# Kernel optimization log

Measured on AMD Instinct MI355X. Metric: run time of the kernel, lower is better.

The kernel has to match this reference:

```python
import jax, jax.numpy as jnp
import numpy as np

N_NODES = 50000
N_EDGES = 800000
B = 512
DIM_IN = 128
D2 = 200
D3 = 200
GC1 = 100
DG = 20
DH = 64
H1 = 128
H2 = 32
BN_EPS = 1e-5


def _lin_init(k, fan_in, fan_out):
    s = 1.0 / np.sqrt(fan_in)
    kw, kb = jax.random.split(k)
    W = jax.random.uniform(kw, (fan_in, fan_out), jnp.float32, -s, s)
    b = jax.random.uniform(kb, (fan_out,), jnp.float32, -s, s)
    return W, b


def setup_inputs() -> dict:
    key = jax.random.key(0)
    ks = jax.random.split(key, 16)
    feat = jax.random.normal(ks[0], (N_NODES, DIM_IN), jnp.float32)
    desc_2d = jax.random.normal(ks[1], (B, D2), jnp.float32)
    desc_3d = jax.random.normal(ks[2], (B, D3), jnp.float32)
    src = jax.random.randint(ks[3], (N_EDGES,), 0, N_NODES, jnp.int32)
    dst = jax.random.randint(ks[4], (N_EDGES,), 0, N_NODES, jnp.int32)
    graph_id = jnp.sort(jax.random.randint(ks[5], (N_NODES,), 0, B, jnp.int32))
    gc1_W, gc1_b = _lin_init(ks[6], DIM_IN, GC1)
    gc2_W, gc2_b = _lin_init(ks[7], GC1, DG)
    pg_W, pg_b = _lin_init(ks[8], DG, DH)
    p2_W, p2_b = _lin_init(ks[9], D2, DH)
    # xavier_uniform for W2
    lim = np.sqrt(6.0 / (DH + DH))
    W2 = jax.random.uniform(ks[10], (DH, DH), jnp.float32, -lim, lim)
    fusion_dim = (DG + 1) * (D2 + 1)
    fc1_W, fc1_b = _lin_init(ks[11], fusion_dim, H1)
    fc2_W, fc2_b = _lin_init(ks[12], H1, H2)
    fc3_W, fc3_b = _lin_init(ks[13], H2, 1)
    return {
        'feat': feat, 'desc_2d': desc_2d, 'desc_3d': desc_3d,
        'gc1_W': gc1_W, 'gc1_b': gc1_b, 'gc2_W': gc2_W, 'gc2_b': gc2_b,
        'pg_W': pg_W, 'pg_b': pg_b, 'p2_W': p2_W, 'p2_b': p2_b, 'W2': W2,
        'fc1_W': fc1_W, 'fc1_b': fc1_b, 'fc2_W': fc2_W, 'fc2_b': fc2_b,
        'fc3_W': fc3_W, 'fc3_b': fc3_b,
        'bn1_g': jnp.ones((H1,), jnp.float32), 'bn1_b': jnp.zeros((H1,), jnp.float32),
        'bn2_g': jnp.ones((H2,), jnp.float32), 'bn2_b': jnp.zeros((H2,), jnp.float32),
        'src': src, 'dst': dst, 'graph_id': graph_id,
    }


def _gcn(h, src, dst, W, b):
    # copy_u -> mean over incoming mailbox -> linear apply
    agg = jax.ops.segment_sum(h[src], dst, num_segments=N_NODES)
    deg = jax.ops.segment_sum(jnp.ones((src.shape[0],), h.dtype), dst, num_segments=N_NODES)
    h_mean = agg / jnp.maximum(deg, 1.0)[:, None]  # zero in-degree -> 0 (DGL default)
    return h_mean @ W + b


def _bn(x, g, b):
    mu = x.mean(0)
    var = x.var(0)
    return (x - mu) * jax.lax.rsqrt(var + BN_EPS) * g + b


def reference(feat, desc_2d, desc_3d, gc1_W, gc1_b, gc2_W, gc2_b,
              pg_W, pg_b, p2_W, p2_b, W2,
              fc1_W, fc1_b, fc2_W, fc2_b, fc3_W, fc3_b,
              bn1_g, bn1_b, bn2_g, bn2_b, src, dst, graph_id):
    h = jax.nn.relu(_gcn(feat, src, dst, gc1_W, gc1_b))          # [N, 100]
    h = jax.nn.relu(_gcn(h, src, dst, gc2_W, gc2_b))             # [N, 20]
    # dgl.mean_nodes: per-graph mean of node features
    cnt = jax.ops.segment_sum(jnp.ones((N_NODES,), h.dtype), graph_id, num_segments=B)
    hg = jax.ops.segment_sum(h, graph_id, num_segments=B) / jnp.maximum(cnt, 1.0)[:, None]  # [B, 20]
    h_g = hg @ pg_W + pg_b                                        # [B, 64]
    h_d = desc_2d @ p2_W + p2_b                                   # [B, 64]
    s = ((h_g @ W2) * h_d).sum(-1)                                # [B]
    a = jax.nn.sigmoid(s)[:, None]                                # [B, 1]
    ones = jnp.ones((B, 1), hg.dtype)
    hg1 = jnp.concatenate([hg, ones], axis=1)                     # [B, 21]
    d1 = jnp.concatenate([a * desc_2d, ones], axis=1)             # [B, 201]
    fusion = (hg1[:, :, None] * d1[:, None, :]).reshape(B, -1)    # [B, 21*201]
    out = jax.nn.relu(_bn(fusion @ fc1_W + fc1_b, bn1_g, bn1_b))
    out = jax.nn.relu(_bn(out @ fc2_W + fc2_b, bn2_g, bn2_b))
    return out @ fc3_W + fc3_b                                    # [B, 1]
```

## Files before the change

### kernel.cpp

```cpp
#include <hip/hip_runtime.h>

#define NN 50000
#define NE 800000
#define NB 512
#define DIN 128
#define DD2 200
#define C1 100
#define C2 20
#define DHH 64
#define HH1 128
#define HH2 32
#define KD 201
#define KDP 204
#define NU 2688
#define SCB 196
#define NCT 7
#define NTILE 3125
#define GB1 782
#define FPB 3125
#define FCB 672
#define PS1 128
#define SLOT 32
#define OVFCAP 8192
#define CSTR 16

typedef short sh8 __attribute__((ext_vector_type(8)));
typedef float f32x4 __attribute__((ext_vector_type(4)));

__device__ __forceinline__ unsigned short f2bf(float x) {
    unsigned u = __float_as_uint(x);
    unsigned r = (u + 0x7fffu + ((u >> 16) & 1u)) >> 16;
    return (unsigned short)r;
}
__device__ __forceinline__ float bf_lo(unsigned u) { return __uint_as_float(u << 16); }
__device__ __forceinline__ float bf_hi(unsigned u) { return __uint_as_float(u & 0xffff0000u); }

__global__ void k_packB_init(const float* __restrict__ W, unsigned short* __restrict__ Bf,
                             int* __restrict__ cnt, float* __restrict__ hgs,
                             int* __restrict__ ovfc) {
    int idx = blockIdx.x * 256 + threadIdx.x;
    if (idx < NCT * 4 * 64) {
        int lane = idx & 63;
        int kc = (idx >> 6) & 3;
        int ct = idx >> 8;
        int col = ct * 16 + (lane & 15);
        int k0 = kc * 32 + (lane >> 4) * 8;
        unsigned short* outp = Bf + (size_t)idx * 8;
        #pragma unroll
        for (int e = 0; e < 8; ++e) {
            float v = (col < C1) ? W[(k0 + e) * C1 + col] : 0.f;
            outp[e] = f2bf(v);
        }
    }
    for (int i = idx; i < NN * CSTR; i += SCB * 256) cnt[i] = 0;
    if (idx < NB * C2) hgs[idx] = 0.f;
    if (idx == 0) *ovfc = 0;
}

__global__ __launch_bounds__(256) void k_front(const float* __restrict__ feat,
                                               const unsigned short* __restrict__ Bf,
                                               unsigned char* __restrict__ t1f8,
                                               const int* __restrict__ src,
                                               const int* __restrict__ dst,
                                               int* __restrict__ cnt,
                                               unsigned short* __restrict__ epad,
                                               int2* __restrict__ ovf,
                                               int* __restrict__ ovfc,
                                               const float* __restrict__ desc2d,
                                               const float* __restrict__ W1,
                                               float* __restrict__ V) {
    __shared__ float smem[7168];
    const int tid = threadIdx.x;

    if (blockIdx.x >= GB1 + FCB) {
        int e = (blockIdx.x - GB1 - FCB) * 256 + tid;
        if (e < NE) {
            int d = dst[e], s = src[e];
            int slot = atomicAdd(&cnt[d * CSTR], 1);
            if (slot < SLOT) {
                epad[(size_t)d * SLOT + slot] = (unsigned short)s;
            } else {
                int o = atomicAdd(ovfc, 1);
                if (o < OVFCAP) ovf[o] = make_int2(d, s);
            }
        }
        return;
    }

    if (blockIdx.x < GB1) {
        sh8* sB = (sh8*)smem;
        {
            const uint4* srcp = (const uint4*)Bf;
            uint4* dstp = (uint4*)smem;
            for (int i = tid; i < NCT * 4 * 64; i += 256) dstp[i] = srcp[i];
        }
        __syncthreads();
        const int w = tid >> 6, lane = tid & 63;
        const int ri = lane & 15;
        const int kg = lane >> 4;
        int tile = blockIdx.x * 4 + w;
        if (tile < NTILE) {
            const int n = tile * 16 + ri;
            f32x4 acc[NCT];
            #pragma unroll
            for (int ct = 0; ct < NCT; ++ct) acc[ct] = (f32x4){0.f, 0.f, 0.f, 0.f};
            #pragma unroll
            for (int kc = 0; kc < 4; ++kc) {
                const float* ap = feat + (size_t)n * DIN + kc * 32 + kg * 8;
                float4 a0 = *(const float4*)ap;
                float4 a1 = *(const float4*)(ap + 4);
                union { sh8 v; unsigned short u[8]; } af;
                af.u[0] = f2bf(a0.x); af.u[1] = f2bf(a0.y);
                af.u[2] = f2bf(a0.z); af.u[3] = f2bf(a0.w);
                af.u[4] = f2bf(a1.x); af.u[5] = f2bf(a1.y);
                af.u[6] = f2bf(a1.z); af.u[7] = f2bf(a1.w);
                #pragma unroll
                for (int ct = 0; ct < NCT; ++ct)
                    acc[ct] = __builtin_amdgcn_mfma_f32_16x16x32_bf16(
                        af.v, sB[(ct * 4 + kc) * 64 + lane], acc[ct], 0, 0, 0);
            }
            const int rbase = tile * 16 + kg * 4;
            #pragma unroll
            for (int ct = 0; ct < NCT; ++ct) {
                int col = ct * 16 + ri;
                if (col < C1) {
                    #pragma unroll
                    for (int r = 0; r < 4; ++r) {
                        int pk = __builtin_amdgcn_cvt_pk_fp8_f32(acc[ct][r], acc[ct][r], 0, false);
                        t1f8[(size_t)(rbase + r) * PS1 + col] = (unsigned char)(pk & 0xFF);
                    }
                }
            }
        }
        return;
    }

    {
        float (*S)[KDP] = (float(*)[KDP])smem;
        int fid = blockIdx.x - GB1;
        const int i = fid / 32;
        const int rem = fid % 32;
        const int bt = rem >> 1;
        const int half = rem & 1;
        for (int idx = tid; idx < 32 * 50; idx += 256) {
            int r = idx / 50, c4 = idx % 50;
            *(float4*)&S[r][c4 * 4] =
                *(const float4*)(desc2d + (size_t)(bt * 32 + r) * DD2 + c4 * 4);
        }
        __syncthreads();
        const int c = tid & 31;
        const int rg = tid >> 5;
        float acc[4][2];
        #pragma unroll
        for (int r = 0; r < 4; ++r) { acc[r][0] = 0.f; acc[r][1] = 0.f; }
        const float* Wb = W1 + (size_t)i * (KD * HH1) + half * 64 + c;
        for (int k = 0; k < 200; k += 4) {
            const float* Wk = Wb + (size_t)k * HH1;
            float w0[2], w1[2], w2[2], w3[2];
            #pragma unroll
            for (int m = 0; m < 2; ++m) {
                w0[m] = Wk[32 * m];
                w1[m] = Wk[HH1 + 32 * m];
                w2[m] = Wk[2 * HH1 + 32 * m];
                w3[m] = Wk[3 * HH1 + 32 * m];
            }
            #pragma unroll
            for (int r = 0; r < 4; ++r) {
                float4 a4 = *(const float4*)&S[rg * 4 + r][k];
                #pragma unroll
                for (int m = 0; m < 2; ++m)
                    acc[r][m] += a4.x * w0[m] + a4.y * w1[m] + a4.z * w2[m] + a4.w * w3[m];
            }
        }
        #pragma unroll
        for (int r = 0; r < 4; ++r) {
            int b = bt * 32 + rg * 4 + r;
            float* Vr = V + (size_t)b * NU + i * HH1 + half * 64 + c;
            Vr[0] = acc[r][0];
            Vr[32] = acc[r][1];
        }
    }
}

__global__ __launch_bounds__(256) void k_agg1(const unsigned char* __restrict__ t1f8,
                                              const int* __restrict__ cnt,
                                              const unsigned short* __restrict__ epad,
                                              const int2* __restrict__ ovf,
                                              const int* __restrict__ ovfc,
                                              const float* __restrict__ b1,
                                              unsigned* __restrict__ h1b) {
    const int tid = threadIdx.x;
    const int w = tid >> 6, l = tid & 63;
    const int n = blockIdx.x * 4 + w;
    if (n >= NN || l >= 50) return;
    const int deg = cnt[n * CSTR];
    const int m = deg < SLOT ? deg : SLOT;
    const unsigned short* ep = epad + (size_t)n * SLOT;
    const int co = 2 * l;
    float acc0 = 0.f, acc1 = 0.f;
    int e = 0;
    for (; e + 7 < m; e += 8) {
        int s0 = ep[e],     s1 = ep[e + 1], s2 = ep[e + 2], s3 = ep[e + 3];
        int s4 = ep[e + 4], s5 = ep[e + 5], s6 = ep[e + 6], s7 = ep[e + 7];
        int u0 = *(const unsigned short*)(t1f8 + (size_t)s0 * PS1 + co);
        int u1 = *(const unsigned short*)(t1f8 + (size_t)s1 * PS1 + co);
        int u2 = *(const unsigned short*)(t1f8 + (size_t)s2 * PS1 + co);
        int u3 = *(const unsigned short*)(t1f8 + (size_t)s3 * PS1 + co);
        int u4 = *(const unsigned short*)(t1f8 + (size_t)s4 * PS1 + co);
        int u5 = *(const unsigned short*)(t1f8 + (size_t)s5 * PS1 + co);
        int u6 = *(const unsigned short*)(t1f8 + (size_t)s6 * PS1 + co);
        int u7 = *(const unsigned short*)(t1f8 + (size_t)s7 * PS1 + co);
        acc0 += __builtin_amdgcn_cvt_f32_fp8(u0, 0); acc1 += __builtin_amdgcn_cvt_f32_fp8(u0, 1);
        acc0 += __builtin_amdgcn_cvt_f32_fp8(u1, 0); acc1 += __builtin_amdgcn_cvt_f32_fp8(u1, 1);
        acc0 += __builtin_amdgcn_cvt_f32_fp8(u2, 0); acc1 += __builtin_amdgcn_cvt_f32_fp8(u2, 1);
        acc0 += __builtin_amdgcn_cvt_f32_fp8(u3, 0); acc1 += __builtin_amdgcn_cvt_f32_fp8(u3, 1);
        acc0 += __builtin_amdgcn_cvt_f32_fp8(u4, 0); acc1 += __builtin_amdgcn_cvt_f32_fp8(u4, 1);
        acc0 += __builtin_amdgcn_cvt_f32_fp8(u5, 0); acc1 += __builtin_amdgcn_cvt_f32_fp8(u5, 1);
        acc0 += __builtin_amdgcn_cvt_f32_fp8(u6, 0); acc1 += __builtin_amdgcn_cvt_f32_fp8(u6, 1);
        acc0 += __builtin_amdgcn_cvt_f32_fp8(u7, 0); acc1 += __builtin_amdgcn_cvt_f32_fp8(u7, 1);
    }
    for (; e < m; ++e) {
        int u = *(const unsigned short*)(t1f8 + (size_t)ep[e] * PS1 + co);
        acc0 += __builtin_amdgcn_cvt_f32_fp8(u, 0);
        acc1 += __builtin_amdgcn_cvt_f32_fp8(u, 1);
    }
    if (deg > SLOT) {
        int novf = *ovfc; novf = novf < OVFCAP ? novf : OVFCAP;
        for (int j2 = 0; j2 < novf; ++j2) {
            int2 p = ovf[j2];
            if (p.x == n) {
                int u = *(const unsigned short*)(t1f8 + (size_t)p.y * PS1 + co);
                acc0 += __builtin_amdgcn_cvt_f32_fp8(u, 0);
                acc1 += __builtin_amdgcn_cvt_f32_fp8(u, 1);
            }
        }
    }
    float d = (float)(deg > 0 ? deg : 1);
    float v0 = fmaxf(acc0 / d + b1[co], 0.f);
    float v1 = fmaxf(acc1 / d + b1[co + 1], 0.f);
    h1b[(size_t)n * 50 + l] = (unsigned)f2bf(v0) | ((unsigned)f2bf(v1) << 16);
}

__global__ void k_gemm2(const unsigned* __restrict__ h1b, const float* __restrict__ W,
                        unsigned* __restrict__ t2b) {
    __shared__ float sW[C1 * C2];
    __shared__ float sr[16][C1];
    __shared__ float sc[16][C2];
    for (int idx = threadIdx.x; idx < C1 * C2; idx += 320) sW[idx] = W[idx];
    int ln = threadIdx.x / C2, j = threadIdx.x % C2;
    int n0 = blockIdx.x * 16;
    for (int idx = threadIdx.x; idx < 16 * 50; idx += 320) {
        int r = idx / 50, c = idx % 50;
        int n = n0 + r;
        unsigned u = (n < NN) ? h1b[(size_t)n * 50 + c] : 0u;
        sr[r][2 * c] = bf_lo(u);
        sr[r][2 * c + 1] = bf_hi(u);
    }
    __syncthreads();
    if (ln < 16) {
        float acc = 0.f;
        #pragma unroll 4
        for (int k = 0; k < C1; ++k) acc += sr[ln][k] * sW[k * C2 + j];
        sc[ln][j] = acc;
    }
    __syncthreads();
    for (int idx = threadIdx.x; idx < 16 * 10; idx += 320) {
        int r = idx / 10, jp = idx % 10;
        int n = n0 + r;
        if (n < NN)
            t2b[(size_t)n * 10 + jp] =
                (unsigned)f2bf(sc[r][2 * jp]) | ((unsigned)f2bf(sc[r][2 * jp + 1]) << 16);
    }
}

__global__ void k_agg2p(const unsigned* __restrict__ t2b, const int* __restrict__ cnt,
                        const unsigned short* __restrict__ epad, const int2* __restrict__ ovf,
                        const int* __restrict__ ovfc, const float* __restrict__ bias,
                        const int* __restrict__ gid, float* __restrict__ hgs) {
    int ln = threadIdx.x / C2, c = threadIdx.x % C2;
    if (ln >= 12) return;
    int n = blockIdx.x * 12 + ln;
    if (n >= NN) return;
    const int deg = cnt[n * CSTR];
    const int m = deg < SLOT ? deg : SLOT;
    const unsigned short* ep = epad + (size_t)n * SLOT;
    const int jp = c >> 1, hi = c & 1;
    float acc = 0.f;
    int e = 0;
    for (; e + 3 < m; e += 4) {
        int s0 = ep[e], s1 = ep[e + 1], s2 = ep[e + 2], s3 = ep[e + 3];
        unsigned u0 = t2b[(size_t)s0 * 10 + jp];
        unsigned u1 = t2b[(size_t)s1 * 10 + jp];
        unsigned u2 = t2b[(size_t)s2 * 10 + jp];
        unsigned u3 = t2b[(size_t)s3 * 10 + jp];
        acc += hi ? bf_hi(u0) : bf_lo(u0);
        acc += hi ? bf_hi(u1) : bf_lo(u1);
        acc += hi ? bf_hi(u2) : bf_lo(u2);
        acc += hi ? bf_hi(u3) : bf_lo(u3);
    }
    for (; e < m; ++e) {
        unsigned u = t2b[(size_t)ep[e] * 10 + jp];
        acc += hi ? bf_hi(u) : bf_lo(u);
    }
    if (deg > SLOT) {
        int novf = *ovfc; novf = novf < OVFCAP ? novf : OVFCAP;
        for (int j2 = 0; j2 < novf; ++j2) {
            int2 p = ovf[j2];
            if (p.x == n) {
                unsigned u = t2b[(size_t)p.y * 10 + jp];
                acc += hi ? bf_hi(u) : bf_lo(u);
            }
        }
    }
    float d = (float)(deg > 0 ? deg : 1);
    float v = acc / d + bias[c];
    v = v > 0.f ? v : 0.f;
    atomicAdd(&hgs[gid[n] * C2 + c], v);
}

__global__ __launch_bounds__(128) void k_hfc1(const float* __restrict__ hgs,
                                              const int* __restrict__ gid,
                                              const float* __restrict__ desc2d,
                                              const float* __restrict__ pgW,
                                              const float* __restrict__ pgb,
                                              const float* __restrict__ p2W,
                                              const float* __restrict__ p2b,
                                              const float* __restrict__ W2,
                                              const float* __restrict__ V,
                                              const float* __restrict__ W1,
                                              float* __restrict__ o1) {
    __shared__ float shg[C2];
    __shared__ float sg[DHH];
    __shared__ float sa;
    const int b = blockIdx.x, tid = threadIdx.x;
    if (tid < C2) {
        int lo = 0, hi = NN;
        while (lo < hi) { int m = (lo + hi) >> 1; if (gid[m] < b) lo = m + 1; else hi = m; }
        int lo2 = lo, hi2 = NN;
        while (lo2 < hi2) { int m = (lo2 + hi2) >> 1; if (gid[m] < b + 1) lo2 = m + 1; else hi2 = m; }
        float dcnt = (float)(lo2 - lo);
        if (dcnt < 1.f) dcnt = 1.f;
        shg[tid] = hgs[b * C2 + tid] / dcnt;
    }
    __syncthreads();
    float hdj = 0.f;
    if (tid < DHH) {
        float hgj = pgb[tid];
        #pragma unroll
        for (int k = 0; k < C2; ++k) hgj += shg[k] * pgW[k * DHH + tid];
        hdj = p2b[tid];
        #pragma unroll 4
        for (int k = 0; k < DD2; ++k) hdj += desc2d[b * DD2 + k] * p2W[k * DHH + tid];
        sg[tid] = hgj;
    }
    __syncthreads();
    if (tid < DHH) {
        float tj = 0.f;
        #pragma unroll 4
        for (int k = 0; k < DHH; ++k) tj += sg[k] * W2[k * DHH + tid];
        float v = tj * hdj;
        #pragma unroll
        for (int off = 32; off; off >>= 1) v += __shfl_xor(v, off, 64);
        if (tid == 0) sa = 1.f / (1.f + expf(-v));
    }
    __syncthreads();
    const int j = tid;
    const float* Vb = V + (size_t)b * NU + j;
    const float* WL = W1 + (size_t)200 * HH1 + j;
    float sv = Vb[20 * HH1];
    float sw = WL[(size_t)20 * KD * HH1];
    #pragma unroll
    for (int i = 0; i < 20; ++i) {
        float h = shg[i];
        sv += h * Vb[i * HH1];
        sw += h * WL[(size_t)i * KD * HH1];
    }
    o1[b * HH1 + j] = sa * sv + sw;
}

__global__ __launch_bounds__(128) void k_fc2s(const float* __restrict__ o1,
                                              const float* __restrict__ g,
                                              const float* __restrict__ beta,
                                              const float* __restrict__ W,
                                              float* __restrict__ o2) {
    __shared__ float r[HH1];
    __shared__ float part[4][HH2];
    const int tid = threadIdx.x;
    float s = 0.f, s2 = 0.f;
    for (int b = 0; b < NB; ++b) {
        float v = o1[b * HH1 + tid];
        s += v; s2 += v * v;
    }
    float mu = s / NB;
    float rstd = rsqrtf(s2 / NB - mu * mu + 1e-5f);
    float scale = rstd * g[tid];
    float shift = beta[tid] - mu * scale;
    const int m = tid & 31, p = tid >> 5;
    for (int q = 0; q < 4; ++q) {
        int b = blockIdx.x * 4 + q;
        float v = o1[b * HH1 + tid];
        __syncthreads();
        r[tid] = fmaxf(v * scale + shift, 0.f);
        __syncthreads();
        float acc = 0.f;
        #pragma unroll 4
        for (int j = p * 32; j < p * 32 + 32; ++j) acc += r[j] * W[j * HH2 + m];
        part[p][m] = acc;
        __syncthreads();
        if (tid < HH2) o2[b * HH2 + tid] = part[0][tid] + part[1][tid] + part[2][tid] + part[3][tid];
    }
}

__global__ __launch_bounds__(512) void k_finals(const float* __restrict__ o2,
                                                const float* __restrict__ g,
                                                const float* __restrict__ beta,
                                                const float* __restrict__ W3,
                                                const float* __restrict__ b3,
                                                float* __restrict__ out) {
    __shared__ float ps[16][HH2], ps2[16][HH2];
    __shared__ float sscale[HH2], sshift[HH2];
    const int tid = threadIdx.x;
    const int gq = tid >> 5, m = tid & 31;
    float s = 0.f, s2 = 0.f;
    for (int rr = 0; rr < 32; ++rr) {
        float v = o2[(gq * 32 + rr) * HH2 + m];
        s += v; s2 += v * v;
    }
    ps[gq][m] = s; ps2[gq][m] = s2;
    __syncthreads();
    if (tid < HH2) {
        float ts = 0.f, ts2 = 0.f;
        #pragma unroll
        for (int q = 0; q < 16; ++q) { ts += ps[q][tid]; ts2 += ps2[q][tid]; }
        float mu = ts / NB;
        float rstd = rsqrtf(ts2 / NB - mu * mu + 1e-5f);
        float scale = rstd * g[tid];
        sscale[tid] = scale;
        sshift[tid] = beta[tid] - mu * scale;
    }
    __syncthreads();
    float acc = b3[0];
    #pragma unroll 4
    for (int mm = 0; mm < HH2; ++mm) {
        float v = o2[tid * HH2 + mm];
        acc += fmaxf(v * sscale[mm] + sshift[mm], 0.f) * W3[mm];
    }
    out[tid] = acc;
}

extern "C" void kernel_launch(void* const* d_in, const int* in_sizes, int n_in,
                              void* d_out, int out_size, void* d_ws, size_t ws_size,
                              hipStream_t stream) {
    const float* feat   = (const float*)d_in[0];
    const float* desc2d = (const float*)d_in[1];
    const float* gc1W = (const float*)d_in[3];
    const float* gc1b = (const float*)d_in[4];
    const float* gc2W = (const float*)d_in[5];
    const float* gc2b = (const float*)d_in[6];
    const float* pgW  = (const float*)d_in[7];
    const float* pgb  = (const float*)d_in[8];
    const float* p2W  = (const float*)d_in[9];
    const float* p2b  = (const float*)d_in[10];
    const float* W2   = (const float*)d_in[11];
    const float* fc1W = (const float*)d_in[12];
    const float* fc2W = (const float*)d_in[14];
    const float* fc3W = (const float*)d_in[16];
    const float* fc3b = (const float*)d_in[17];
    const float* bn1g = (const float*)d_in[18];
    const float* bn1b = (const float*)d_in[19];
    const float* bn2g = (const float*)d_in[20];
    const float* bn2b = (const float*)d_in[21];
    const int* src = (const int*)d_in[22];
    const int* dst = (const int*)d_in[23];
    const int* gid = (const int*)d_in[24];
    float* out = (float*)d_out;

    char* ws = (char*)d_ws;
    size_t off = 0;
    auto alloc = [&](size_t nb) {
        void* p = ws + off;
        off = (off + nb + 255) & ~(size_t)255;
        return p;
    };
    unsigned char* t1f8 = (unsigned char*)alloc((size_t)NN * PS1);
    unsigned* h1b = (unsigned*)alloc((size_t)NN * 50 * 4);
    unsigned* t2b = (unsigned*)alloc((size_t)NN * 10 * 4);
    int* cnt_in  = (int*)alloc((size_t)NN * CSTR * 4);
    unsigned short* epad = (unsigned short*)alloc((size_t)NN * SLOT * 2);
    int2* ovf    = (int2*)alloc((size_t)OVFCAP * 8);
    int* ovfc    = (int*)alloc(256);
    unsigned short* Bf = (unsigned short*)alloc((size_t)NCT * 4 * 64 * 16);
    float* V     = (float*)alloc((size_t)NB * NU * 4);
    float* hgs   = (float*)alloc((size_t)NB * C2 * 4);
    float* o1    = (float*)alloc((size_t)NB * HH1 * 4);
    float* o2    = (float*)alloc((size_t)NB * HH2 * 4);

    k_packB_init<<<SCB, 256, 0, stream>>>(gc1W, Bf, cnt_in, hgs, ovfc);
    k_front<<<GB1 + FCB + FPB, 256, 0, stream>>>(feat, Bf, t1f8, src, dst, cnt_in,
                                                 epad, ovf, ovfc, desc2d, fc1W, V);

    k_agg1<<<(NN + 3) / 4, 256, 0, stream>>>(t1f8, cnt_in, epad, ovf, ovfc, gc1b, h1b);
    k_gemm2<<<(NN + 15) / 16, 320, 0, stream>>>(h1b, gc2W, t2b);
    k_agg2p<<<(NN + 11) / 12, 256, 0, stream>>>(t2b, cnt_in, epad, ovf, ovfc, gc2b, gid, hgs);

    k_hfc1<<<NB, 128, 0, stream>>>(hgs, gid, desc2d, pgW, pgb, p2W, p2b, W2, V, fc1W, o1);
    k_fc2s<<<NB / 4, 128, 0, stream>>>(o1, bn1g, bn1b, fc2W, o2);
    k_finals<<<1, 512, 0, stream>>>(o2, bn2g, bn2b, fc3W, fc3b, out);
}
```

Before: 182.6 us.

## Fuse layer-1 neighbor aggregation with layer-2 GEMM in one kernel

Merges the first GCN aggregation kernel and the 100x20 projection GEMM into one kernel. Each 1024-thread block aggregates 16 nodes into shared memory, then multiplies them by the shared-memory copy of W2 and writes the bf16 outputs. This removes the h1b intermediate buffer's global write and read and one kernel launch. The cost is large blocks with a barrier, which may hurt occupancy and latency hiding in the gather-bound aggregation, and each block reloads W2.

```diff
diff --git a/kernel.cpp b/kernel.cpp
--- a/kernel.cpp
+++ b/kernel.cpp
@@ -182,94 +182,81 @@
     }
 }
 
-__global__ __launch_bounds__(256) void k_agg1(const unsigned char* __restrict__ t1f8,
-                                              const int* __restrict__ cnt,
-                                              const unsigned short* __restrict__ epad,
-                                              const int2* __restrict__ ovf,
-                                              const int* __restrict__ ovfc,
-                                              const float* __restrict__ b1,
-                                              unsigned* __restrict__ h1b) {
+__global__ __launch_bounds__(1024) void k_agg1g2(const unsigned char* __restrict__ t1f8,
+                                                 const int* __restrict__ cnt,
+                                                 const unsigned short* __restrict__ epad,
+                                                 const int2* __restrict__ ovf,
+                                                 const int* __restrict__ ovfc,
+                                                 const float* __restrict__ b1,
+                                                 const float* __restrict__ W2,
+                                                 unsigned* __restrict__ t2b) {
+    __shared__ float sW2[C1 * C2];
+    __shared__ float sh1[16][C1];
+    __shared__ float sc[16][C2];
     const int tid = threadIdx.x;
+    for (int idx = tid; idx < C1 * C2; idx += 1024) sW2[idx] = W2[idx];
     const int w = tid >> 6, l = tid & 63;
-    const int n = blockIdx.x * 4 + w;
-    if (n >= NN || l >= 50) return;
-    const int deg = cnt[n * CSTR];
-    const int m = deg < SLOT ? deg : SLOT;
-    const unsigned short* ep = epad + (size_t)n * SLOT;
-    const int co = 2 * l;
-    float acc0 = 0.f, acc1 = 0.f;
-    int e = 0;
-    for (; e + 7 < m; e += 8) {
-        int s0 = ep[e],     s1 = ep[e + 1], s2 = ep[e + 2], s3 = ep[e + 3];
-        int s4 = ep[e + 4], s5 = ep[e + 5], s6 = ep[e + 6], s7 = ep[e + 7];
-        int u0 = *(const unsigned short*)(t1f8 + (size_t)s0 * PS1 + co);
-        int u1 = *(const unsigned short*)(t1f8 + (size_t)s1 * PS1 + co);
-        int u2 = *(const unsigned short*)(t1f8 + (size_t)s2 * PS1 + co);
-        int u3 = *(const unsigned short*)(t1f8 + (size_t)s3 * PS1 + co);
-        int u4 = *(const unsigned short*)(t1f8 + (size_t)s4 * PS1 + co);
-        int u5 = *(const unsigned short*)(t1f8 + (size_t)s5 * PS1 + co);
-        int u6 = *(const unsigned short*)(t1f8 + (size_t)s6 * PS1 + co);
-        int u7 = *(const unsigned short*)(t1f8 + (size_t)s7 * PS1 + co);
-        acc0 += __builtin_amdgcn_cvt_f32_fp8(u0, 0); acc1 += __builtin_amdgcn_cvt_f32_fp8(u0, 1);
-        acc0 += __builtin_amdgcn_cvt_f32_fp8(u1, 0); acc1 += __builtin_amdgcn_cvt_f32_fp8(u1, 1);
-        acc0 += __builtin_amdgcn_cvt_f32_fp8(u2, 0); acc1 += __builtin_amdgcn_cvt_f32_fp8(u2, 1);
-        acc0 += __builtin_amdgcn_cvt_f32_fp8(u3, 0); acc1 += __builtin_amdgcn_cvt_f32_fp8(u3, 1);
-        acc0 += __builtin_amdgcn_cvt_f32_fp8(u4, 0); acc1 += __builtin_amdgcn_cvt_f32_fp8(u4, 1);
-        acc0 += __builtin_amdgcn_cvt_f32_fp8(u5, 0); acc1 += __builtin_amdgcn_cvt_f32_fp8(u5, 1);
-        acc0 += __builtin_amdgcn_cvt_f32_fp8(u6, 0); acc1 += __builtin_amdgcn_cvt_f32_fp8(u6, 1);
-        acc0 += __builtin_amdgcn_cvt_f32_fp8(u7, 0); acc1 += __builtin_amdgcn_cvt_f32_fp8(u7, 1);
-    }
-    for (; e < m; ++e) {
-        int u = *(const unsigned short*)(t1f8 + (size_t)ep[e] * PS1 + co);
-        acc0 += __builtin_amdgcn_cvt_f32_fp8(u, 0);
-        acc1 += __builtin_amdgcn_cvt_f32_fp8(u, 1);
-    }
-    if (deg > SLOT) {
-        int novf = *ovfc; novf = novf < OVFCAP ? novf : OVFCAP;
-        for (int j2 = 0; j2 < novf; ++j2) {
-            int2 p = ovf[j2];
-            if (p.x == n) {
-                int u = *(const unsigned short*)(t1f8 + (size_t)p.y * PS1 + co);
-                acc0 += __builtin_amdgcn_cvt_f32_fp8(u, 0);
-                acc1 += __builtin_amdgcn_cvt_f32_fp8(u, 1);
-            }
-        }
-    }
-    float d = (float)(deg > 0 ? deg : 1);
-    float v0 = fmaxf(acc0 / d + b1[co], 0.f);
-    float v1 = fmaxf(acc1 / d + b1[co + 1], 0.f);
-    h1b[(size_t)n * 50 + l] = (unsigned)f2bf(v0) | ((unsigned)f2bf(v1) << 16);
-}
-
-__global__ void k_gemm2(const unsigned* __restrict__ h1b, const float* __restrict__ W,
-                        unsigned* __restrict__ t2b) {
-    __shared__ float sW[C1 * C2];
-    __shared__ float sr[16][C1];
-    __shared__ float sc[16][C2];
-    for (int idx = threadIdx.x; idx < C1 * C2; idx += 320) sW[idx] = W[idx];
-    int ln = threadIdx.x / C2, j = threadIdx.x % C2;
-    int n0 = blockIdx.x * 16;
-    for (int idx = threadIdx.x; idx < 16 * 50; idx += 320) {
-        int r = idx / 50, c = idx % 50;
-        int n = n0 + r;
-        unsigned u = (n < NN) ? h1b[(size_t)n * 50 + c] : 0u;
-        sr[r][2 * c] = bf_lo(u);
-        sr[r][2 * c + 1] = bf_hi(u);
-    }
-    __syncthreads();
-    if (ln < 16) {
+    const int n = blockIdx.x * 16 + w;
+    if (l < 50) {
+        const int deg = cnt[n * CSTR];
+        const int m = deg < SLOT ? deg : SLOT;
+        const unsigned short* ep = epad + (size_t)n * SLOT;
+        const int co = 2 * l;
+        float acc0 = 0.f, acc1 = 0.f;
+        int e = 0;
+        for (; e + 7 < m; e += 8) {
+            int s0 = ep[e],     s1 = ep[e + 1], s2 = ep[e + 2], s3 = ep[e + 3];
+            int s4 = ep[e + 4], s5 = ep[e + 5], s6 = ep[e + 6], s7 = ep[e + 7];
+            int u0 = *(const unsigned short*)(t1f8 + (size_t)s0 * PS1 + co);
+            int u1 = *(const unsigned short*)(t1f8 + (size_t)s1 * PS1 + co);
+            int u2 = *(const unsigned short*)(t1f8 + (size_t)s2 * PS1 + co);
+            int u3 = *(const unsigned short*)(t1f8 + (size_t)s3 * PS1 + co);
+            int u4 = *(const unsigned short*)(t1f8 + (size_t)s4 * PS1 + co);
+            int u5 = *(const unsigned short*)(t1f8 + (size_t)s5 * PS1 + co);
+            int u6 = *(const unsigned short*)(t1f8 + (size_t)s6 * PS1 + co);
+            int u7 = *(const unsigned short*)(t1f8 + (size_t)s7 * PS1 + co);
+            acc0 += __builtin_amdgcn_cvt_f32_fp8(u0, 0); acc1 += __builtin_amdgcn_cvt_f32_fp8(u0, 1);
+            acc0 += __builtin_amdgcn_cvt_f32_fp8(u1, 0); acc1 += __builtin_amdgcn_cvt_f32_fp8(u1, 1);
+            acc0 += __builtin_amdgcn_cvt_f32_fp8(u2, 0); acc1 += __builtin_amdgcn_cvt_f32_fp8(u2, 1);
+            acc0 += __builtin_amdgcn_cvt_f32_fp8(u3, 0); acc1 += __builtin_amdgcn_cvt_f32_fp8(u3, 1);
+            acc0 += __builtin_amdgcn_cvt_f32_fp8(u4, 0); acc1 += __builtin_amdgcn_cvt_f32_fp8(u4, 1);
+            acc0 += __builtin_amdgcn_cvt_f32_fp8(u5, 0); acc1 += __builtin_amdgcn_cvt_f32_fp8(u5, 1);
+            acc0 += __builtin_amdgcn_cvt_f32_fp8(u6, 0); acc1 += __builtin_amdgcn_cvt_f32_fp8(u6, 1);
+            acc0 += __builtin_amdgcn_cvt_f32_fp8(u7, 0); acc1 += __builtin_amdgcn_cvt_f32_fp8(u7, 1);
+        }
+        for (; e < m; ++e) {
+            int u = *(const unsigned short*)(t1f8 + (size_t)ep[e] * PS1 + co);
+            acc0 += __builtin_amdgcn_cvt_f32_fp8(u, 0);
+            acc1 += __builtin_amdgcn_cvt_f32_fp8(u, 1);
+        }
+        if (deg > SLOT) {
+            int novf = *ovfc; novf = novf < OVFCAP ? novf : OVFCAP;
+            for (int j2 = 0; j2 < novf; ++j2) {
+                int2 p = ovf[j2];
+                if (p.x == n) {
+                    int u = *(const unsigned short*)(t1f8 + (size_t)p.y * PS1 + co);
+                    acc0 += __builtin_amdgcn_cvt_f32_fp8(u, 0);
+                    acc1 += __builtin_amdgcn_cvt_f32_fp8(u, 1);
+                }
+            }
+        }
+        float d = (float)(deg > 0 ? deg : 1);
+        sh1[w][2 * l]     = fmaxf(acc0 / d + b1[2 * l], 0.f);
+        sh1[w][2 * l + 1] = fmaxf(acc1 / d + b1[2 * l + 1], 0.f);
+    }
+    __syncthreads();
+    if (tid < 16 * C2) {
+        int ln = tid / C2, j = tid % C2;
         float acc = 0.f;
         #pragma unroll 4
-        for (int k = 0; k < C1; ++k) acc += sr[ln][k] * sW[k * C2 + j];
+        for (int k = 0; k < C1; ++k) acc += sh1[ln][k] * sW2[k * C2 + j];
         sc[ln][j] = acc;
     }
     __syncthreads();
-    for (int idx = threadIdx.x; idx < 16 * 10; idx += 320) {
-        int r = idx / 10, jp = idx % 10;
-        int n = n0 + r;
-        if (n < NN)
-            t2b[(size_t)n * 10 + jp] =
-                (unsigned)f2bf(sc[r][2 * jp]) | ((unsigned)f2bf(sc[r][2 * jp + 1]) << 16);
+    if (tid < 16 * 10) {
+        int r = tid / 10, jp = tid % 10;
+        t2b[(size_t)(blockIdx.x * 16 + r) * 10 + jp] =
+            (unsigned)f2bf(sc[r][2 * jp]) | ((unsigned)f2bf(sc[r][2 * jp + 1]) << 16);
     }
 }
 
@@ -483,7 +470,6 @@
         return p;
     };
     unsigned char* t1f8 = (unsigned char*)alloc((size_t)NN * PS1);
-    unsigned* h1b = (unsigned*)alloc((size_t)NN * 50 * 4);
     unsigned* t2b = (unsigned*)alloc((size_t)NN * 10 * 4);
     int* cnt_in  = (int*)alloc((size_t)NN * CSTR * 4);
     unsigned short* epad = (unsigned short*)alloc((size_t)NN * SLOT * 2);
@@ -499,8 +485,7 @@
     k_front<<<GB1 + FCB + FPB, 256, 0, stream>>>(feat, Bf, t1f8, src, dst, cnt_in,
                                                  epad, ovf, ovfc, desc2d, fc1W, V);
 
-    k_agg1<<<(NN + 3) / 4, 256, 0, stream>>>(t1f8, cnt_in, epad, ovf, ovfc, gc1b, h1b);
-    k_gemm2<<<(NN + 15) / 16, 320, 0, stream>>>(h1b, gc2W, t2b);
+    k_agg1g2<<<NTILE, 1024, 0, stream>>>(t1f8, cnt_in, epad, ovf, ovfc, gc1b, gc2W, t2b);
     k_agg2p<<<(NN + 11) / 12, 256, 0, stream>>>(t2b, cnt_in, epad, ovf, ovfc, gc2b, gid, hgs);
 
     k_hfc1<<<NB, 128, 0, stream>>>(hgs, gid, desc2d, pgW, pgb, p2W, p2b, W2, V, fc1W, o1);
```

After: 182.6 us, median of 2. About the same (-0.0%).
